# Optimization experiments

Measured on AMD Instinct MI355X. Metric: run time of the kernel, lower is better.

## Reference

```python
import jax, jax.numpy as jnp
import numpy as np

MAX_DISP = 4  # matches init_kwargs max_displacement


def setup_inputs() -> dict:
    key = jax.random.key(0)
    k1, k2 = jax.random.split(key)
    B, C, H, W = 8, 256, 128, 128
    in1 = jax.random.normal(k1, (B, C, H, W), dtype=jnp.float32)
    in2 = jax.random.normal(k2, (B, C, H, W), dtype=jnp.float32)
    return {"in1": in1, "in2": in2}


def reference(in1, in2):
    d = MAX_DISP
    B, C, H, W = in1.shape
    # zero-pad in2 by d on both spatial dims (ConstantPad2d(d, 0))
    in2_pad = jnp.pad(in2, ((0, 0), (0, 0), (d, d), (d, d)))
    # torch.meshgrid default 'ij' indexing + reshape(-1): dy varies slow, dx fast
    outs = [
        jnp.sum(in1 * jax.lax.dynamic_slice(in2_pad, (0, 0, dy, dx), (B, C, H, W)), axis=1)
        for dy in range(2 * d + 1)
        for dx in range(2 * d + 1)
    ]
    return jnp.stack(outs, axis=1)  # [B, (2d+1)^2, H, W]
```

## Files before the change

### kernel.cpp

```cpp
#include <hip/hip_runtime.h>


constexpr int Bn = 8, Cn = 256, Hn = 128, Wn = 128, HW = Hn * Wn;
constexpr int Dd = 4, ND = 9;
constexpr int KC = 16;
constexpr int NP = KC / 2;
constexpr int NT = 576;
constexpr int W2 = Wn + 8;

typedef __fp16 h2v __attribute__((ext_vector_type(2)));

static __device__ __forceinline__ unsigned packh2(float a, float b) {
  h2v h = __builtin_amdgcn_cvt_pkrtz(a, b);
  return __builtin_bit_cast(unsigned, h);
}

static __device__ __forceinline__ float dot2(unsigned a, unsigned b, float c) {
#if __has_builtin(__builtin_amdgcn_fdot2)
  return __builtin_amdgcn_fdot2(__builtin_bit_cast(h2v, a),
                                __builtin_bit_cast(h2v, b), c, false);
#else
  h2v ha = __builtin_bit_cast(h2v, a), hb = __builtin_bit_cast(h2v, b);
  return c + (float)ha.x * (float)hb.x + (float)ha.y * (float)hb.y;
#endif
}

__global__ __launch_bounds__(NT) void corr_kernel(
    const float* __restrict__ in1, const float* __restrict__ in2,
    float* __restrict__ out)
{
  __shared__ __align__(16) unsigned s1h[NP][2][Wn];
  __shared__ __align__(16) unsigned s2h[NP][10][W2];

  int bid = blockIdx.x;
  bid = (bid & 7) * 64 + (bid >> 3);
  const int b  = bid >> 6;
  const int y0 = (bid & 63) << 1;

  const int tid  = threadIdx.x;
  const int dy   = tid >> 6;
  const int lane = tid & 63;
  const int row  = lane >> 5;
  const int xq   = (lane & 31) << 2;

  const size_t base = (size_t)b * Cn * HW;

  for (int i = tid * 4; i < NP * 10 * W2; i += NT * 4)
    *(uint4*)(&s2h[0][0][0] + i) = uint4{0, 0, 0, 0};

  float4 acc[ND];
#pragma unroll
  for (int dx = 0; dx < ND; ++dx) acc[dx] = float4{0.f, 0.f, 0.f, 0.f};

  const int srow = dy + row;

  for (int c0 = 0; c0 < Cn; c0 += KC) {
    __syncthreads();

    for (int i = tid; i < NP * 2 * 32; i += NT) {
      const int p  = i >> 6;
      const int yy = (i >> 5) & 1;
      const int gx = (i & 31) << 2;
      const float* s = in1 + base + (size_t)(c0 + 2 * p) * HW + (y0 + yy) * Wn + gx;
      const float4 f0 = *(const float4*)s;
      const float4 f1 = *(const float4*)(s + HW);
      uint4 w;
      w.x = packh2(f0.x, f1.x); w.y = packh2(f0.y, f1.y);
      w.z = packh2(f0.z, f1.z); w.w = packh2(f0.w, f1.w);
      *(uint4*)&s1h[p][yy][gx] = w;
    }

    for (int i = tid; i < NP * 10 * 32; i += NT) {
      const int p   = i / 320;
      const int rem = i - p * 320;
      const int r   = rem >> 5;
      const int gx  = (rem & 31) << 2;
      const int gy  = y0 + r - Dd;
      const bool ok = (unsigned)gy < (unsigned)Hn;
      const int gyc = ok ? gy : 0;
      const float* s = in2 + base + (size_t)(c0 + 2 * p) * HW + (size_t)gyc * Wn + gx;
      const float4 f0 = *(const float4*)s;
      const float4 f1 = *(const float4*)(s + HW);
      uint4 w;
      w.x = packh2(f0.x, f1.x); w.y = packh2(f0.y, f1.y);
      w.z = packh2(f0.z, f1.z); w.w = packh2(f0.w, f1.w);
      if (!ok) w = uint4{0, 0, 0, 0};
      *(uint4*)&s2h[p][r][4 + gx] = w;
    }
    __syncthreads();

#pragma unroll
    for (int kc = 0; kc < NP; ++kc) {
      const unsigned* bp = &s2h[kc][srow][xq];
      const uint4 b0 = *(const uint4*)bp;
      const uint4 b1 = *(const uint4*)(bp + 4);
      const uint4 b2 = *(const uint4*)(bp + 8);
      const uint4 av = *(const uint4*)&s1h[kc][row][xq];
      const unsigned bb[12] = {b0.x, b0.y, b0.z, b0.w, b1.x, b1.y,
                               b1.z, b1.w, b2.x, b2.y, b2.z, b2.w};
      const unsigned aa[4] = {av.x, av.y, av.z, av.w};
#pragma unroll
      for (int dx = 0; dx < ND; ++dx) {
        acc[dx].x = dot2(aa[0], bb[0 + dx], acc[dx].x);
        acc[dx].y = dot2(aa[1], bb[1 + dx], acc[dx].y);
        acc[dx].z = dot2(aa[2], bb[2 + dx], acc[dx].z);
        acc[dx].w = dot2(aa[3], bb[3 + dx], acc[dx].w);
      }
    }
  }

#pragma unroll
  for (int dx = 0; dx < ND; ++dx) {
    const size_t o =
        (((size_t)b * (ND * ND) + dy * ND + dx) * Hn + (y0 + row)) * Wn + xq;
    *(float4*)&out[o] = acc[dx];
  }
}

extern "C" void kernel_launch(void* const* d_in, const int* in_sizes, int n_in,
                              void* d_out, int out_size, void* d_ws, size_t ws_size,
                              hipStream_t stream) {
  const float* in1 = (const float*)d_in[0];
  const float* in2 = (const float*)d_in[1];
  float* out = (float*)d_out;
  dim3 grid(Bn * (Hn / 2));
  dim3 block(NT);
  hipLaunchKernelGGL(corr_kernel, grid, block, 0, stream, in1, in2, out);
}
```

Baseline: 111.0 us.

## Split channel reduction across two blocks and combine with atomic adds

Doubles the grid by splitting the 256-channel reduction into two halves handled by separate blocks, each accumulating partial correlations. Outputs are zeroed with a memset and partial sums are combined via scalar float atomicAdd. This aims to raise parallelism and latency hiding, at the cost of an extra memset pass, atomic traffic on the large output, and non-deterministic summation order.

```diff
diff --git a/kernel.cpp b/kernel.cpp
--- a/kernel.cpp
+++ b/kernel.cpp
@@ -3,8 +3,8 @@
 
 constexpr int Bn = 8, Cn = 256, Hn = 128, Wn = 128, HW = Hn * Wn;
 constexpr int Dd = 4, ND = 9;
-constexpr int KC = 16;
-constexpr int NP = KC / 2;
+constexpr int CHB = 128;
+constexpr int KC = 16, NP = KC / 2;
 constexpr int NT = 576;
 constexpr int W2 = Wn + 8;
 
@@ -32,18 +32,18 @@
   __shared__ __align__(16) unsigned s1h[NP][2][Wn];
   __shared__ __align__(16) unsigned s2h[NP][10][W2];
 
-  int bid = blockIdx.x;
-  bid = (bid & 7) * 64 + (bid >> 3);
-  const int b  = bid >> 6;
-  const int y0 = (bid & 63) << 1;
+  const int o  = blockIdx.x;
+  const int b  = o & 7;
+  const int ch = (o >> 3) & 1;
+  const int y0 = (o >> 4) << 1;
 
   const int tid  = threadIdx.x;
   const int dy   = tid >> 6;
   const int lane = tid & 63;
   const int row  = lane >> 5;
-  const int xq   = (lane & 31) << 2;
-
-  const size_t base = (size_t)b * Cn * HW;
+  const int x0   = (lane & 31) << 2;
+  const int srow = dy + row;
+  const size_t base = (size_t)b * Cn * HW + (size_t)ch * CHB * HW;
 
   for (int i = tid * 4; i < NP * 10 * W2; i += NT * 4)
     *(uint4*)(&s2h[0][0][0] + i) = uint4{0, 0, 0, 0};
@@ -52,9 +52,7 @@
 #pragma unroll
   for (int dx = 0; dx < ND; ++dx) acc[dx] = float4{0.f, 0.f, 0.f, 0.f};
 
-  const int srow = dy + row;
-
-  for (int c0 = 0; c0 < Cn; c0 += KC) {
+  for (int c0 = 0; c0 < CHB; c0 += KC) {
     __syncthreads();
 
     for (int i = tid; i < NP * 2 * 32; i += NT) {
@@ -91,29 +89,32 @@
 
 #pragma unroll
     for (int kc = 0; kc < NP; ++kc) {
-      const unsigned* bp = &s2h[kc][srow][xq];
+      const unsigned* bp = &s2h[kc][srow][x0];
       const uint4 b0 = *(const uint4*)bp;
       const uint4 b1 = *(const uint4*)(bp + 4);
       const uint4 b2 = *(const uint4*)(bp + 8);
-      const uint4 av = *(const uint4*)&s1h[kc][row][xq];
+      const uint4 av = *(const uint4*)&s1h[kc][row][x0];
       const unsigned bb[12] = {b0.x, b0.y, b0.z, b0.w, b1.x, b1.y,
                                b1.z, b1.w, b2.x, b2.y, b2.z, b2.w};
       const unsigned aa[4] = {av.x, av.y, av.z, av.w};
 #pragma unroll
       for (int dx = 0; dx < ND; ++dx) {
-        acc[dx].x = dot2(aa[0], bb[0 + dx], acc[dx].x);
-        acc[dx].y = dot2(aa[1], bb[1 + dx], acc[dx].y);
-        acc[dx].z = dot2(aa[2], bb[2 + dx], acc[dx].z);
-        acc[dx].w = dot2(aa[3], bb[3 + dx], acc[dx].w);
+        acc[dx].x = dot2(aa[0], bb[dx + 0], acc[dx].x);
+        acc[dx].y = dot2(aa[1], bb[dx + 1], acc[dx].y);
+        acc[dx].z = dot2(aa[2], bb[dx + 2], acc[dx].z);
+        acc[dx].w = dot2(aa[3], bb[dx + 3], acc[dx].w);
       }
     }
   }
 
 #pragma unroll
   for (int dx = 0; dx < ND; ++dx) {
-    const size_t o =
-        (((size_t)b * (ND * ND) + dy * ND + dx) * Hn + (y0 + row)) * Wn + xq;
-    *(float4*)&out[o] = acc[dx];
+    const size_t oo =
+        (((size_t)b * (ND * ND) + dy * ND + dx) * Hn + (y0 + row)) * Wn + x0;
+    atomicAdd(&out[oo + 0], acc[dx].x);
+    atomicAdd(&out[oo + 1], acc[dx].y);
+    atomicAdd(&out[oo + 2], acc[dx].z);
+    atomicAdd(&out[oo + 3], acc[dx].w);
   }
 }
 
@@ -123,7 +124,8 @@
   const float* in1 = (const float*)d_in[0];
   const float* in2 = (const float*)d_in[1];
   float* out = (float*)d_out;
-  dim3 grid(Bn * (Hn / 2));
+  hipMemsetAsync(d_out, 0, (size_t)out_size * sizeof(float), stream);
+  dim3 grid(Bn * 2 * (Hn / 2));
   dim3 block(NT);
   hipLaunchKernelGGL(corr_kernel, grid, block, 0, stream, in1, in2, out);
 }
```

Result: slower. 344.9 us (+210.6%).

## Double-buffer in2 tiles in LDS and read in1 directly from global

Applied to the files above, without the earlier changes.

Replaces the single-buffered LDS staging with two in2 buffers, so the next channel chunk is prefetched while the current one is computed and only one barrier per chunk remains. in1 is no longer staged in LDS; each thread loads its own in1 values from global and software-prefetches the next channel pair. The channel chunk shrinks from 16 to 8 and only the halo columns are zeroed. Each thread now reloads in1 from global redundantly, since the 9 dy waves load the same values, and the smaller chunk doubles the loop iterations.

```diff
diff --git a/kernel.cpp b/kernel.cpp
--- a/kernel.cpp
+++ b/kernel.cpp
@@ -3,10 +3,11 @@
 
 constexpr int Bn = 8, Cn = 256, Hn = 128, Wn = 128, HW = Hn * Wn;
 constexpr int Dd = 4, ND = 9;
-constexpr int KC = 16;
-constexpr int NP = KC / 2;
+constexpr int KC = 8, NP = KC / 2;
+constexpr int NCH = Cn / KC;
 constexpr int NT = 576;
 constexpr int W2 = Wn + 8;
+constexpr int BUFSZ = NP * 10 * W2;
 
 typedef __fp16 h2v __attribute__((ext_vector_type(2)));
 
@@ -29,8 +30,7 @@
     const float* __restrict__ in1, const float* __restrict__ in2,
     float* __restrict__ out)
 {
-  __shared__ __align__(16) unsigned s1h[NP][2][Wn];
-  __shared__ __align__(16) unsigned s2h[NP][10][W2];
+  __shared__ __align__(16) unsigned lds2[2 * BUFSZ];
 
   int bid = blockIdx.x;
   bid = (bid & 7) * 64 + (bid >> 3);
@@ -41,78 +41,98 @@
   const int dy   = tid >> 6;
   const int lane = tid & 63;
   const int row  = lane >> 5;
-  const int xq   = (lane & 31) << 2;
-
+  const int x0   = (lane & 31) << 2;
+  const int srow = dy + row;
   const size_t base = (size_t)b * Cn * HW;
 
-  for (int i = tid * 4; i < NP * 10 * W2; i += NT * 4)
-    *(uint4*)(&s2h[0][0][0] + i) = uint4{0, 0, 0, 0};
+  for (int i = tid; i < 2 * NP * 10 * 2; i += NT) {
+    const int bf = i / (NP * 10 * 2), rem = i - bf * (NP * 10 * 2);
+    const int pr = rem >> 1, side = rem & 1;
+    *(uint4*)&lds2[bf * BUFSZ + pr * W2 + side * 132] = uint4{0, 0, 0, 0};
+  }
 
   float4 acc[ND];
 #pragma unroll
   for (int dx = 0; dx < ND; ++dx) acc[dx] = float4{0.f, 0.f, 0.f, 0.f};
 
-  const int srow = dy + row;
+  const float* ip = in1 + base + (size_t)(y0 + row) * Wn + x0;
 
-  for (int c0 = 0; c0 < Cn; c0 += KC) {
-    __syncthreads();
+  for (int i = tid; i < NP * 10 * 32; i += NT) {
+    const int p   = i / 320;
+    const int rem = i - p * 320;
+    const int r   = rem >> 5;
+    const int gx  = (rem & 31) << 2;
+    const int gy  = y0 + r - Dd;
+    const bool ok = (unsigned)gy < (unsigned)Hn;
+    const float* s = in2 + base + (size_t)(2 * p) * HW +
+                     (size_t)(ok ? gy : 0) * Wn + gx;
+    const float4 f0 = *(const float4*)s;
+    const float4 f1 = *(const float4*)(s + HW);
+    uint4 w;
+    w.x = packh2(f0.x, f1.x); w.y = packh2(f0.y, f1.y);
+    w.z = packh2(f0.z, f1.z); w.w = packh2(f0.w, f1.w);
+    if (!ok) w = uint4{0, 0, 0, 0};
+    *(uint4*)&lds2[(p * 10 + r) * W2 + 4 + gx] = w;
+  }
+  __syncthreads();
 
-    for (int i = tid; i < NP * 2 * 32; i += NT) {
-      const int p  = i >> 6;
-      const int yy = (i >> 5) & 1;
-      const int gx = (i & 31) << 2;
-      const float* s = in1 + base + (size_t)(c0 + 2 * p) * HW + (y0 + yy) * Wn + gx;
-      const float4 f0 = *(const float4*)s;
-      const float4 f1 = *(const float4*)(s + HW);
-      uint4 w;
-      w.x = packh2(f0.x, f1.x); w.y = packh2(f0.y, f1.y);
-      w.z = packh2(f0.z, f1.z); w.w = packh2(f0.w, f1.w);
-      *(uint4*)&s1h[p][yy][gx] = w;
+  for (int c = 0; c < NCH; ++c) {
+    if (c + 1 < NCH) {
+      const unsigned nb = ((c + 1) & 1) * BUFSZ;
+      const float* sp = in2 + base + (size_t)(c + 1) * KC * HW;
+      for (int i = tid; i < NP * 10 * 32; i += NT) {
+        const int p   = i / 320;
+        const int rem = i - p * 320;
+        const int r   = rem >> 5;
+        const int gx  = (rem & 31) << 2;
+        const int gy  = y0 + r - Dd;
+        const bool ok = (unsigned)gy < (unsigned)Hn;
+        const float* s = sp + (size_t)(2 * p) * HW +
+                         (size_t)(ok ? gy : 0) * Wn + gx;
+        const float4 f0 = *(const float4*)s;
+        const float4 f1 = *(const float4*)(s + HW);
+        uint4 w;
+        w.x = packh2(f0.x, f1.x); w.y = packh2(f0.y, f1.y);
+        w.z = packh2(f0.z, f1.z); w.w = packh2(f0.w, f1.w);
+        if (!ok) w = uint4{0, 0, 0, 0};
+        *(uint4*)&lds2[nb + (p * 10 + r) * W2 + 4 + gx] = w;
+      }
     }
 
-    for (int i = tid; i < NP * 10 * 32; i += NT) {
-      const int p   = i / 320;
-      const int rem = i - p * 320;
-      const int r   = rem >> 5;
-      const int gx  = (rem & 31) << 2;
-      const int gy  = y0 + r - Dd;
-      const bool ok = (unsigned)gy < (unsigned)Hn;
-      const int gyc = ok ? gy : 0;
-      const float* s = in2 + base + (size_t)(c0 + 2 * p) * HW + (size_t)gyc * Wn + gx;
-      const float4 f0 = *(const float4*)s;
-      const float4 f1 = *(const float4*)(s + HW);
-      uint4 w;
-      w.x = packh2(f0.x, f1.x); w.y = packh2(f0.y, f1.y);
-      w.z = packh2(f0.z, f1.z); w.w = packh2(f0.w, f1.w);
-      if (!ok) w = uint4{0, 0, 0, 0};
-      *(uint4*)&s2h[p][r][4 + gx] = w;
-    }
-    __syncthreads();
-
+    const unsigned* bufp = &lds2[(c & 1) * BUFSZ];
+    const float* cp = ip + (size_t)c * KC * HW;
+    float4 A0 = *(const float4*)cp;
+    float4 A1 = *(const float4*)(cp + HW);
 #pragma unroll
-    for (int kc = 0; kc < NP; ++kc) {
-      const unsigned* bp = &s2h[kc][srow][xq];
+    for (int p = 0; p < NP; ++p) {
+      const unsigned aa[4] = {packh2(A0.x, A1.x), packh2(A0.y, A1.y),
+                              packh2(A0.z, A1.z), packh2(A0.w, A1.w)};
+      if (p < NP - 1) {
+        const float* np = cp + (size_t)(2 * p + 2) * HW;
+        A0 = *(const float4*)np;
+        A1 = *(const float4*)(np + HW);
+      }
+      const unsigned* bp = bufp + (p * 10 + srow) * W2 + x0;
       const uint4 b0 = *(const uint4*)bp;
       const uint4 b1 = *(const uint4*)(bp + 4);
       const uint4 b2 = *(const uint4*)(bp + 8);
-      const uint4 av = *(const uint4*)&s1h[kc][row][xq];
       const unsigned bb[12] = {b0.x, b0.y, b0.z, b0.w, b1.x, b1.y,
                                b1.z, b1.w, b2.x, b2.y, b2.z, b2.w};
-      const unsigned aa[4] = {av.x, av.y, av.z, av.w};
 #pragma unroll
       for (int dx = 0; dx < ND; ++dx) {
-        acc[dx].x = dot2(aa[0], bb[0 + dx], acc[dx].x);
-        acc[dx].y = dot2(aa[1], bb[1 + dx], acc[dx].y);
-        acc[dx].z = dot2(aa[2], bb[2 + dx], acc[dx].z);
-        acc[dx].w = dot2(aa[3], bb[3 + dx], acc[dx].w);
+        acc[dx].x = dot2(aa[0], bb[dx + 0], acc[dx].x);
+        acc[dx].y = dot2(aa[1], bb[dx + 1], acc[dx].y);
+        acc[dx].z = dot2(aa[2], bb[dx + 2], acc[dx].z);
+        acc[dx].w = dot2(aa[3], bb[dx + 3], acc[dx].w);
       }
     }
+    __syncthreads();
   }
 
 #pragma unroll
   for (int dx = 0; dx < ND; ++dx) {
     const size_t o =
-        (((size_t)b * (ND * ND) + dy * ND + dx) * Hn + (y0 + row)) * Wn + xq;
+        (((size_t)b * (ND * ND) + dy * ND + dx) * Hn + (y0 + row)) * Wn + x0;
     *(float4*)&out[o] = acc[dx];
   }
 }
```

Result: slower. 126.1 us (+13.6%).
